# Kernel tuning notes

Measured on AMD Instinct MI355X. Metric: run time of the kernel, lower is better.

The kernel has to match this reference:

```python
import jax, jax.numpy as jnp
import numpy as np

HEAD_NUM = 8
QKV_DIM = 16
SQRT_EMBEDDING_DIM = 11.313708498984761  # sqrt(128)
LOGIT_CLIPPING = 10.0


def _reshape_by_heads(x):
    # x: [B, n, H*D] -> [B, H, n, D]
    B, n, _ = x.shape
    return x.reshape(B, n, HEAD_NUM, QKV_DIM).transpose(0, 2, 1, 3)


def setup_inputs() -> dict:
    key = jax.random.key(0)
    ks = jax.random.split(key, 12)
    B, P, N, E = 64, 500, 501, 128
    HD = HEAD_NUM * QKV_DIM
    s = 0.05
    return {
        "encoded_last_node": jax.random.normal(ks[0], (B, P, E), jnp.float32),
        "load": jax.random.uniform(ks[1], (B, P), jnp.float32),
        "ninf_mask": jnp.zeros((B, P, N), jnp.float32),
        "encoded_nodes": jax.random.normal(ks[2], (B, N, E), jnp.float32),
        "Wq_last": jax.random.normal(ks[3], (E + 1, HD), jnp.float32) * s,
        "Wk": jax.random.normal(ks[4], (E, HD), jnp.float32) * s,
        "Wv": jax.random.normal(ks[5], (E, HD), jnp.float32) * s,
        "mhc_W": jax.random.normal(ks[6], (HD, E), jnp.float32) * s,
        "mhc_b": jax.random.normal(ks[7], (E,), jnp.float32) * s,
        "new": jax.random.normal(ks[8], (B, HD, HD), jnp.float32) * s,
        "new_bias": jax.random.normal(ks[9], (B, 1, HD), jnp.float32) * s,
        "new_2": jax.random.normal(ks[10], (B, HD, HD), jnp.float32) * s,
        "new_bias_2": jax.random.normal(ks[11], (B, 1, HD), jnp.float32) * s,
    }


def reference(encoded_last_node, load, ninf_mask, encoded_nodes,
              Wq_last, Wk, Wv, mhc_W, mhc_b,
              new, new_bias, new_2, new_bias_2):
    B, P, E = encoded_last_node.shape
    # set_kv
    k = _reshape_by_heads(encoded_nodes @ Wk)            # [B,H,N,D]
    v = _reshape_by_heads(encoded_nodes @ Wv)            # [B,H,N,D]
    single_head_key = encoded_nodes.transpose(0, 2, 1)   # [B,E,N]

    # q from (last node embedding, load)
    input_cat = jnp.concatenate([encoded_last_node, load[:, :, None]], axis=2)  # [B,P,E+1]
    q = _reshape_by_heads(input_cat @ Wq_last)           # [B,H,P,D]

    # multi-head attention
    score = jnp.einsum('bhpd,bhnd->bhpn', q, k) / jnp.sqrt(jnp.float32(QKV_DIM))
    score = score + ninf_mask[:, None, :, :]
    attn = jax.nn.softmax(score, axis=3)
    out = jnp.einsum('bhpn,bhnd->bhpd', attn, v)         # [B,H,P,D]
    out_concat = out.transpose(0, 2, 1, 3).reshape(B, P, HEAD_NUM * QKV_DIM)

    # per-batch affine + relu + residual
    residual = out_concat
    h = jax.nn.relu(jnp.matmul(out_concat, new) + new_bias)
    h = jnp.matmul(h, new_2) + new_bias_2 + residual

    mh_atten_out = h @ mhc_W + mhc_b                     # [B,P,E]

    score2 = jnp.matmul(mh_atten_out, single_head_key)   # [B,P,N]
    score_clipped = LOGIT_CLIPPING * jnp.tanh(score2 / SQRT_EMBEDDING_DIM)
    probs = jax.nn.softmax(score_clipped + ninf_mask, axis=2)
    return probs
```

## Files before the change

kernel.cpp:

```cpp
#include <hip/hip_runtime.h>
#include <hip/hip_bf16.h>
#include <math.h>

typedef float f4 __attribute__((ext_vector_type(4)));

#define BATCH 64
#define PP 500
#define NN 501

__global__ __launch_bounds__(256) void k_proj(
    const float* __restrict__ Xq,
    const float* __restrict__ Ld,
    const float* __restrict__ Xn,
    const float* __restrict__ Wq,
    const float* __restrict__ Wk, const float* __restrict__ Wv,
    float* __restrict__ Q, float* __restrict__ K_, float* __restrict__ V_)
{
  __shared__ float xs[64*132];
  const int t = threadIdx.x;
  const int tr = t >> 5, tc = t & 31;
  if (blockIdx.x < 500) {
    const int r0 = blockIdx.x * 64;
    for (int i = t; i < 64*32; i += 256) {
      int r = i >> 5, k4 = (i & 31) << 2;
      *(f4*)(xs + r*132 + k4) = *(const f4*)(Xq + (size_t)(r0+r)*128 + k4);
    }
    if (t < 64) xs[t*132 + 128] = Ld[r0 + t];
    __syncthreads();
    float acc[8][4];
    #pragma unroll
    for (int i = 0; i < 8; i++)
      #pragma unroll
      for (int c = 0; c < 4; c++) acc[i][c] = 0.f;
    for (int k4 = 0; k4 < 128; k4 += 4) {
      f4 x[8], w[4];
      #pragma unroll
      for (int j = 0; j < 4; j++) w[j] = *(const f4*)(Wq + (size_t)(k4+j)*128 + tc*4);
      #pragma unroll
      for (int i = 0; i < 8; i++) x[i] = *(const f4*)(xs + (tr*8+i)*132 + k4);
      #pragma unroll
      for (int i = 0; i < 8; i++)
        #pragma unroll
        for (int j = 0; j < 4; j++)
          #pragma unroll
          for (int c = 0; c < 4; c++)
            acc[i][c] += x[i][j] * w[j][c];
    }
    {
      f4 w = *(const f4*)(Wq + (size_t)128*128 + tc*4);
      #pragma unroll
      for (int i = 0; i < 8; i++) {
        float xv = xs[(tr*8+i)*132 + 128];
        #pragma unroll
        for (int c = 0; c < 4; c++) acc[i][c] += xv * w[c];
      }
    }
    #pragma unroll
    for (int i = 0; i < 8; i++) {
      f4 o;
      #pragma unroll
      for (int c = 0; c < 4; c++) o[c] = acc[i][c];
      *(f4*)(Q + (size_t)(r0 + tr*8 + i)*128 + tc*4) = o;
    }
  } else {
    const int r0 = (blockIdx.x - 500) * 64;
    for (int i = t; i < 64*32; i += 256) {
      int r = i >> 5, k4 = (i & 31) << 2;
      *(f4*)(xs + r*132 + k4) = *(const f4*)(Xn + (size_t)(r0+r)*128 + k4);
    }
    __syncthreads();
    float accK[8][4], accV[8][4];
    #pragma unroll
    for (int i = 0; i < 8; i++)
      #pragma unroll
      for (int c = 0; c < 4; c++) { accK[i][c] = 0.f; accV[i][c] = 0.f; }
    for (int k4 = 0; k4 < 128; k4 += 4) {
      f4 x[8], wk[4], wv[4];
      #pragma unroll
      for (int j = 0; j < 4; j++) {
        wk[j] = *(const f4*)(Wk + (size_t)(k4+j)*128 + tc*4);
        wv[j] = *(const f4*)(Wv + (size_t)(k4+j)*128 + tc*4);
      }
      #pragma unroll
      for (int i = 0; i < 8; i++) x[i] = *(const f4*)(xs + (tr*8+i)*132 + k4);
      #pragma unroll
      for (int i = 0; i < 8; i++)
        #pragma unroll
        for (int j = 0; j < 4; j++)
          #pragma unroll
          for (int c = 0; c < 4; c++) {
            accK[i][c] += x[i][j] * wk[j][c];
            accV[i][c] += x[i][j] * wv[j][c];
          }
    }
    #pragma unroll
    for (int i = 0; i < 8; i++) {
      f4 ok, ov;
      #pragma unroll
      for (int c = 0; c < 4; c++) { ok[c] = accK[i][c]; ov[c] = accV[i][c]; }
      *(f4*)(K_ + (size_t)(r0 + tr*8 + i)*128 + tc*4) = ok;
      *(f4*)(V_ + (size_t)(r0 + tr*8 + i)*128 + tc*4) = ov;
    }
  }
}

__global__ __launch_bounds__(256, 3) void k_attn(
    const float* __restrict__ Q, const float* __restrict__ K_, const float* __restrict__ V_,
    const float* __restrict__ Msk, float* __restrict__ OC)
{
  __shared__ float ks[32*128];
  __shared__ float vs[32*128];
  __shared__ float mkt[32*64];
  const int blk = blockIdx.x;
  const int b  = blk >> 3;
  const int pt = blk & 7;
  const int p0 = pt * 64;
  const int t = threadIdx.x;
  const int h    = t >> 5;
  const int rowA = t & 31;
  const int rowB = rowA + 32;
  const int pA = p0 + rowA;
  const int pB0 = p0 + rowB;
  const bool bvalid = pB0 < PP;
  const int pB = bvalid ? pB0 : (PP - 1);

  f4 qA0, qA1, qA2, qA3, qB0, qB1, qB2, qB3;
  {
    const float* qa = Q + ((size_t)b*PP + pA)*128 + h*16;
    qA0 = *(const f4*)(qa); qA1 = *(const f4*)(qa+4); qA2 = *(const f4*)(qa+8); qA3 = *(const f4*)(qa+12);
    const float* qb = Q + ((size_t)b*PP + pB)*128 + h*16;
    qB0 = *(const f4*)(qb); qB1 = *(const f4*)(qb+4); qB2 = *(const f4*)(qb+8); qB3 = *(const f4*)(qb+12);
  }

  float mA = -1e30f, lA = 0.f, mB = -1e30f, lB = 0.f;
  f4 oA0 = {0.f,0.f,0.f,0.f}, oA1 = oA0, oA2 = oA0, oA3 = oA0;
  f4 oB0 = oA0, oB1 = oA0, oB2 = oA0, oB3 = oA0;

  const int mr = t >> 3;
  const int nq = (t & 7) << 2;
  const float* gmA = Msk + ((size_t)b*PP + p0 + mr)*NN;
  const float* gmB = Msk + ((size_t)b*PP + min(p0 + mr + 32, PP-1))*NN;

  for (int c0 = 0; c0 < NN; c0 += 32) {
    __syncthreads();
    #pragma unroll
    for (int u = 0; u < 4; u++) {
      int i = t + u*256;
      int n = i >> 5, d4 = (i & 31) << 2;
      int ng = c0 + n;
      f4 kv = {0.f,0.f,0.f,0.f}, vv = {0.f,0.f,0.f,0.f};
      if (ng < NN) {
        kv = *(const f4*)(K_ + ((size_t)b*NN + ng)*128 + d4);
        vv = *(const f4*)(V_ + ((size_t)b*NN + ng)*128 + d4);
      }
      *(f4*)(ks + n*128 + d4) = kv;
      *(f4*)(vs + n*128 + d4) = vv;
    }
    #pragma unroll
    for (int j = 0; j < 4; j++) {
      int nn = c0 + nq + j;
      bool cv = nn < NN;
      float a  = cv ? gmA[nn] : -1e30f;
      float bb = cv ? gmB[nn] : -1e30f;
      mkt[(nq+j)*64 + mr]      = a;
      mkt[(nq+j)*64 + mr + 32] = bb;
    }
    __syncthreads();

    #pragma unroll
    for (int n = 0; n < 32; n++) {
      const float* kf = ks + n*128 + h*16;
      f4 k0 = *(const f4*)(kf);
      f4 k1 = *(const f4*)(kf + 4);
      f4 k2 = *(const f4*)(kf + 8);
      f4 k3 = *(const f4*)(kf + 12);
      float sA = 0.f, sB = 0.f;
      #pragma unroll
      for (int d = 0; d < 4; d++) {
        sA += qA0[d]*k0[d]; sB += qB0[d]*k0[d];
        sA += qA1[d]*k1[d]; sB += qB1[d]*k1[d];
        sA += qA2[d]*k2[d]; sB += qB2[d]*k2[d];
        sA += qA3[d]*k3[d]; sB += qB3[d]*k3[d];
      }
      sA = sA*0.25f + mkt[n*64 + rowA];
      sB = sB*0.25f + mkt[n*64 + rowB];
      if (sA > mA) {
        float cc = __expf(mA - sA); mA = sA; lA *= cc;
        oA0 *= cc; oA1 *= cc; oA2 *= cc; oA3 *= cc;
      }
      if (sB > mB) {
        float cc = __expf(mB - sB); mB = sB; lB *= cc;
        oB0 *= cc; oB1 *= cc; oB2 *= cc; oB3 *= cc;
      }
      float eA = __expf(sA - mA); lA += eA;
      float eB = __expf(sB - mB); lB += eB;
      const float* vf = vs + n*128 + h*16;
      f4 v0 = *(const f4*)(vf);
      f4 v1 = *(const f4*)(vf + 4);
      f4 v2 = *(const f4*)(vf + 8);
      f4 v3 = *(const f4*)(vf + 12);
      oA0 += eA*v0; oA1 += eA*v1; oA2 += eA*v2; oA3 += eA*v3;
      oB0 += eB*v0; oB1 += eB*v1; oB2 += eB*v2; oB3 += eB*v3;
    }
  }

  {
    float inv = 1.f / lA;
    float* orow = OC + ((size_t)b*PP + pA)*128 + h*16;
    *(f4*)(orow)      = oA0 * inv;
    *(f4*)(orow + 4)  = oA1 * inv;
    *(f4*)(orow + 8)  = oA2 * inv;
    *(f4*)(orow + 12) = oA3 * inv;
  }
  if (bvalid) {
    float inv = 1.f / lB;
    float* orow = OC + ((size_t)b*PP + pB)*128 + h*16;
    *(f4*)(orow)      = oB0 * inv;
    *(f4*)(orow + 4)  = oB1 * inv;
    *(f4*)(orow + 8)  = oB2 * inv;
    *(f4*)(orow + 12) = oB3 * inv;
  }
}

__global__ __launch_bounds__(256) void k_ffn(
    const float* __restrict__ OC, const float* __restrict__ Wn, const float* __restrict__ Bn,
    const float* __restrict__ Wn2, const float* __restrict__ Bn2,
    const float* __restrict__ Wm, const float* __restrict__ Bm,
    float* __restrict__ MH)
{
  __shared__ float xs[64*132];
  __shared__ float hs[64*132];
  const int blk = blockIdx.x; const int b = blk >> 3, rb = blk & 7;
  const int r0 = rb*64;
  const int nv = min(64, PP - r0);
  const int t = threadIdx.x;
  const int tr = t >> 5, tc = t & 31;
  const float* ocb = OC + (size_t)b*PP*128;
  for (int i = t; i < 64*32; i += 256) {
    int r = i >> 5, k4 = (i & 31) << 2;
    f4 v = {0.f,0.f,0.f,0.f};
    if (r < nv) v = *(const f4*)(ocb + (size_t)(r0+r)*128 + k4);
    *(f4*)(xs + r*132 + k4) = v;
  }
  __syncthreads();
  {
    const float* W1 = Wn + (size_t)b*16384;
    float acc[8][4];
    #pragma unroll
    for (int i = 0; i < 8; i++)
      #pragma unroll
      for (int c = 0; c < 4; c++) acc[i][c] = 0.f;
    for (int k4 = 0; k4 < 128; k4 += 4) {
      f4 x[8], w[4];
      #pragma unroll
      for (int j = 0; j < 4; j++) w[j] = *(const f4*)(W1 + (size_t)(k4+j)*128 + tc*4);
      #pragma unroll
      for (int i = 0; i < 8; i++) x[i] = *(const f4*)(xs + (tr*8+i)*132 + k4);
      #pragma unroll
      for (int i = 0; i < 8; i++)
        #pragma unroll
        for (int j = 0; j < 4; j++)
          #pragma unroll
          for (int c = 0; c < 4; c++)
            acc[i][c] += x[i][j] * w[j][c];
    }
    f4 b1 = *(const f4*)(Bn + b*128 + tc*4);
    #pragma unroll
    for (int i = 0; i < 8; i++) {
      f4 o;
      #pragma unroll
      for (int c = 0; c < 4; c++) o[c] = fmaxf(acc[i][c] + b1[c], 0.f);
      *(f4*)(hs + (tr*8+i)*132 + tc*4) = o;
    }
  }
  __syncthreads();
  float h2[8][4];
  {
    const float* W2 = Wn2 + (size_t)b*16384;
    float acc[8][4];
    #pragma unroll
    for (int i = 0; i < 8; i++)
      #pragma unroll
      for (int c = 0; c < 4; c++) acc[i][c] = 0.f;
    for (int k4 = 0; k4 < 128; k4 += 4) {
      f4 x[8], w[4];
      #pragma unroll
      for (int j = 0; j < 4; j++) w[j] = *(const f4*)(W2 + (size_t)(k4+j)*128 + tc*4);
      #pragma unroll
      for (int i = 0; i < 8; i++) x[i] = *(const f4*)(hs + (tr*8+i)*132 + k4);
      #pragma unroll
      for (int i = 0; i < 8; i++)
        #pragma unroll
        for (int j = 0; j < 4; j++)
          #pragma unroll
          for (int c = 0; c < 4; c++)
            acc[i][c] += x[i][j] * w[j][c];
    }
    f4 b2 = *(const f4*)(Bn2 + b*128 + tc*4);
    #pragma unroll
    for (int i = 0; i < 8; i++)
      #pragma unroll
      for (int c = 0; c < 4; c++)
        h2[i][c] = acc[i][c] + b2[c] + xs[(tr*8+i)*132 + tc*4 + c];
  }
  __syncthreads();
  #pragma unroll
  for (int i = 0; i < 8; i++) {
    f4 o;
    #pragma unroll
    for (int c = 0; c < 4; c++) o[c] = h2[i][c];
    *(f4*)(hs + (tr*8+i)*132 + tc*4) = o;
  }
  __syncthreads();
  {
    float acc[8][4];
    #pragma unroll
    for (int i = 0; i < 8; i++)
      #pragma unroll
      for (int c = 0; c < 4; c++) acc[i][c] = 0.f;
    for (int k4 = 0; k4 < 128; k4 += 4) {
      f4 x[8], w[4];
      #pragma unroll
      for (int j = 0; j < 4; j++) w[j] = *(const f4*)(Wm + (size_t)(k4+j)*128 + tc*4);
      #pragma unroll
      for (int i = 0; i < 8; i++) x[i] = *(const f4*)(hs + (tr*8+i)*132 + k4);
      #pragma unroll
      for (int i = 0; i < 8; i++)
        #pragma unroll
        for (int j = 0; j < 4; j++)
          #pragma unroll
          for (int c = 0; c < 4; c++)
            acc[i][c] += x[i][j] * w[j][c];
    }
    f4 b3 = *(const f4*)(Bm + tc*4);
    #pragma unroll
    for (int i = 0; i < 8; i++) {
      if (tr*8 + i < nv) {
        f4 o;
        #pragma unroll
        for (int c = 0; c < 4; c++) o[c] = acc[i][c] + b3[c];
        *(f4*)(MH + ((size_t)b*PP + r0 + tr*8 + i)*128 + tc*4) = o;
      }
    }
  }
}

__global__ __launch_bounds__(256, 3) void k_final(
    const float* __restrict__ MH, const float* __restrict__ EN,
    const float* __restrict__ Msk, float* __restrict__ OUT)
{
  __shared__ float ms[32*132];
  __shared__ float es[64*132];
  const int blk = blockIdx.x; const int b = blk >> 4, rb = blk & 15;
  const int r0 = rb*32; const int nv = min(32, PP - r0);
  const int t = threadIdx.x;
  const int tr = t >> 5, tc = t & 31;
  const float* mhb = MH + (size_t)(b*PP + r0)*128;
  for (int i = t; i < 32*32; i += 256) {
    int r = i >> 5, k4 = (i & 31) << 2;
    f4 v = {0.f,0.f,0.f,0.f};
    if (r < nv) v = *(const f4*)(mhb + (size_t)r*128 + k4);
    *(f4*)(ms + r*132 + k4) = v;
  }
  const float* enb = EN + (size_t)b*NN*128;
  float s[8][4][2];
  #pragma unroll
  for (int nt = 0; nt < 8; nt++) {
    const int n0 = nt*64;
    __syncthreads();
    for (int i = t; i < 64*32; i += 256) {
      int n = i >> 5, k4 = (i & 31) << 2;
      f4 v = {0.f,0.f,0.f,0.f};
      if (n0 + n < NN) v = *(const f4*)(enb + (size_t)(n0+n)*128 + k4);
      *(f4*)(es + n*132 + k4) = v;
    }
    __syncthreads();
    float acc[4][2];
    #pragma unroll
    for (int i = 0; i < 4; i++) { acc[i][0] = 0.f; acc[i][1] = 0.f; }
    #pragma unroll 8
    for (int k4 = 0; k4 < 128; k4 += 4) {
      f4 x[4];
      #pragma unroll
      for (int i = 0; i < 4; i++) x[i] = *(const f4*)(ms + (tr*4+i)*132 + k4);
      f4 e0 = *(const f4*)(es + tc*132 + k4);
      f4 e1 = *(const f4*)(es + (tc+32)*132 + k4);
      #pragma unroll
      for (int i = 0; i < 4; i++)
        #pragma unroll
        for (int j = 0; j < 4; j++) {
          acc[i][0] += x[i][j]*e0[j];
          acc[i][1] += x[i][j]*e1[j];
        }
    }
    #pragma unroll
    for (int i = 0; i < 4; i++) {
      s[nt][i][0] = acc[i][0];
      s[nt][i][1] = acc[i][1];
    }
  }
  const float* mkb = Msk + (size_t)(b*PP + r0)*NN;
  #pragma unroll
  for (int nt = 0; nt < 8; nt++)
    #pragma unroll
    for (int i = 0; i < 4; i++)
      #pragma unroll
      for (int c = 0; c < 2; c++) {
        int r = tr*4 + i, n = nt*64 + tc + c*32;
        float val = -INFINITY;
        if (r < nv && n < NN) {
          float E = __expf(s[nt][i][c] * 0.17677669529663687f);
          val = 10.f - 20.f/(E + 1.f) + mkb[(size_t)r*NN + n];
        }
        s[nt][i][c] = val;
      }
  float* ob = OUT + (size_t)(b*PP + r0)*NN;
  #pragma unroll
  for (int i = 0; i < 4; i++) {
    float m = -INFINITY;
    #pragma unroll
    for (int nt = 0; nt < 8; nt++)
      #pragma unroll
      for (int c = 0; c < 2; c++) m = fmaxf(m, s[nt][i][c]);
    #pragma unroll
    for (int o = 16; o > 0; o >>= 1) m = fmaxf(m, __shfl_xor(m, o, 32));
    float l = 0.f;
    #pragma unroll
    for (int nt = 0; nt < 8; nt++)
      #pragma unroll
      for (int c = 0; c < 2; c++) {
        float e_ = __expf(s[nt][i][c] - m);
        s[nt][i][c] = e_;
        l += e_;
      }
    #pragma unroll
    for (int o = 16; o > 0; o >>= 1) l += __shfl_xor(l, o, 32);
    const int r = tr*4 + i;
    if (r < nv) {
      float inv = 1.f / l;
      float* orow = ob + (size_t)r*NN;
      #pragma unroll
      for (int nt = 0; nt < 8; nt++)
        #pragma unroll
        for (int c = 0; c < 2; c++) {
          int n = nt*64 + tc + c*32;
          if (n < NN) orow[n] = s[nt][i][c] * inv;
        }
    }
  }
}

extern "C" void kernel_launch(void* const* d_in, const int* in_sizes, int n_in,
                              void* d_out, int out_size, void* d_ws, size_t ws_size,
                              hipStream_t stream) {
  const float* eln  = (const float*)d_in[0];
  const float* load = (const float*)d_in[1];
  const float* mask = (const float*)d_in[2];
  const float* en   = (const float*)d_in[3];
  const float* Wq   = (const float*)d_in[4];
  const float* Wk   = (const float*)d_in[5];
  const float* Wv   = (const float*)d_in[6];
  const float* Wm   = (const float*)d_in[7];
  const float* Bm   = (const float*)d_in[8];
  const float* Wn   = (const float*)d_in[9];
  const float* Bn   = (const float*)d_in[10];
  const float* Wn2  = (const float*)d_in[11];
  const float* Bn2  = (const float*)d_in[12];
  float* out = (float*)d_out;
  float* ws  = (float*)d_ws;
  float* Q   = ws;
  float* K_  = ws + 4096000;
  float* V_  = ws + 8200192;
  float* OC  = ws + 12304384;
  float* MH  = ws + 16400384;
  hipLaunchKernelGGL(k_proj,  dim3(1001), dim3(256), 0, stream, eln, load, en, Wq, Wk, Wv, Q, K_, V_);
  hipLaunchKernelGGL(k_attn,  dim3(512),  dim3(256), 0, stream, Q, K_, V_, mask, OC);
  hipLaunchKernelGGL(k_ffn,   dim3(512),  dim3(256), 0, stream, OC, Wn, Bn, Wn2, Bn2, Wm, Bm, MH);
  hipLaunchKernelGGL(k_final, dim3(1024), dim3(256), 0, stream, MH, en, mask, out);
}
```

Baseline: 472.0 us.

## Register-prefetch next K/V/mask tile in attention loop and repad mask smem

```diff
diff --git a/kernel.cpp b/kernel.cpp
--- a/kernel.cpp
+++ b/kernel.cpp
@@ -104,23 +104,23 @@
   }
 }
 
-__global__ __launch_bounds__(256, 3) void k_attn(
+__global__ __launch_bounds__(256, 2) void k_attn(
     const float* __restrict__ Q, const float* __restrict__ K_, const float* __restrict__ V_,
     const float* __restrict__ Msk, float* __restrict__ OC)
 {
   __shared__ float ks[32*128];
   __shared__ float vs[32*128];
-  __shared__ float mkt[32*64];
+  __shared__ float mks[64*33];
   const int blk = blockIdx.x;
   const int b  = blk >> 3;
   const int pt = blk & 7;
   const int p0 = pt * 64;
   const int t = threadIdx.x;
-  const int h    = t >> 5;
-  const int rowA = t & 31;
-  const int rowB = rowA + 32;
-  const int pA = p0 + rowA;
-  const int pB0 = p0 + rowB;
+  const int h  = t >> 5;
+  const int rA = t & 31;
+  const int rB = rA + 32;
+  const int pA = p0 + rA;
+  const int pB0 = p0 + rB;
   const bool bvalid = pB0 < PP;
   const int pB = bvalid ? pB0 : (PP - 1);
 
@@ -136,40 +136,64 @@
   f4 oA0 = {0.f,0.f,0.f,0.f}, oA1 = oA0, oA2 = oA0, oA3 = oA0;
   f4 oB0 = oA0, oB1 = oA0, oB2 = oA0, oB3 = oA0;
 
-  const int mr = t >> 3;
-  const int nq = (t & 7) << 2;
-  const float* gmA = Msk + ((size_t)b*PP + p0 + mr)*NN;
-  const float* gmB = Msk + ((size_t)b*PP + min(p0 + mr + 32, PP-1))*NN;
+  const int mr2 = t >> 2;
+  const int nq2 = (t & 3) << 3;
+  const int mrow = min(p0 + mr2, PP - 1);
+  const float* gm = Msk + ((size_t)b*PP + mrow)*NN;
+
+  f4 kpre[4], vpre[4]; float mpre[8];
+  #pragma unroll
+  for (int u = 0; u < 4; u++) {
+    int i = t + u*256;
+    int n = i >> 5, d4 = (i & 31) << 2;
+    kpre[u] = *(const f4*)(K_ + ((size_t)b*NN + n)*128 + d4);
+    vpre[u] = *(const f4*)(V_ + ((size_t)b*NN + n)*128 + d4);
+  }
+  #pragma unroll
+  for (int j = 0; j < 8; j++)
+    mpre[j] = (nq2 + j < NN) ? gm[nq2 + j] : -1e30f;
 
   for (int c0 = 0; c0 < NN; c0 += 32) {
-    __syncthreads();
     #pragma unroll
     for (int u = 0; u < 4; u++) {
       int i = t + u*256;
       int n = i >> 5, d4 = (i & 31) << 2;
-      int ng = c0 + n;
-      f4 kv = {0.f,0.f,0.f,0.f}, vv = {0.f,0.f,0.f,0.f};
-      if (ng < NN) {
-        kv = *(const f4*)(K_ + ((size_t)b*NN + ng)*128 + d4);
-        vv = *(const f4*)(V_ + ((size_t)b*NN + ng)*128 + d4);
-      }
-      *(f4*)(ks + n*128 + d4) = kv;
-      *(f4*)(vs + n*128 + d4) = vv;
-    }
-    #pragma unroll
-    for (int j = 0; j < 4; j++) {
-      int nn = c0 + nq + j;
-      bool cv = nn < NN;
-      float a  = cv ? gmA[nn] : -1e30f;
-      float bb = cv ? gmB[nn] : -1e30f;
-      mkt[(nq+j)*64 + mr]      = a;
-      mkt[(nq+j)*64 + mr + 32] = bb;
+      *(f4*)(ks + n*128 + d4) = kpre[u];
+      *(f4*)(vs + n*128 + d4) = vpre[u];
+    }
+    {
+      float* dm = mks + mr2*33 + nq2;
+      #pragma unroll
+      for (int j = 0; j < 8; j++) dm[j] = mpre[j];
     }
     __syncthreads();
 
+    const int c1 = c0 + 32;
+    if (c1 < NN) {
+      #pragma unroll
+      for (int u = 0; u < 4; u++) {
+        int i = t + u*256;
+        int n = i >> 5, d4 = (i & 31) << 2;
+        int ng = c1 + n;
+        f4 kv = {0.f,0.f,0.f,0.f}, vv = {0.f,0.f,0.f,0.f};
+        if (ng < NN) {
+          kv = *(const f4*)(K_ + ((size_t)b*NN + ng)*128 + d4);
+          vv = *(const f4*)(V_ + ((size_t)b*NN + ng)*128 + d4);
+        }
+        kpre[u] = kv; vpre[u] = vv;
+      }
+      #pragma unroll
+      for (int j = 0; j < 8; j++)
+        mpre[j] = (c1 + nq2 + j < NN) ? gm[c1 + nq2 + j] : -1e30f;
+    }
+
+    const float* ksh = ks + h*16;
+    const float* vsh = vs + h*16;
+    const float* mwA = mks + rA*33;
+    const float* mwB = mks + rB*33;
     #pragma unroll
     for (int n = 0; n < 32; n++) {
-      const float* kf = ks + n*128 + h*16;
+      const float* kf = ksh + n*128;
       f4 k0 = *(const f4*)(kf);
       f4 k1 = *(const f4*)(kf + 4);
       f4 k2 = *(const f4*)(kf + 8);
@@ -182,8 +206,8 @@
         sA += qA2[d]*k2[d]; sB += qB2[d]*k2[d];
         sA += qA3[d]*k3[d]; sB += qB3[d]*k3[d];
       }
-      sA = sA*0.25f + mkt[n*64 + rowA];
-      sB = sB*0.25f + mkt[n*64 + rowB];
+      sA = sA*0.25f + mwA[n];
+      sB = sB*0.25f + mwB[n];
       if (sA > mA) {
         float cc = __expf(mA - sA); mA = sA; lA *= cc;
         oA0 *= cc; oA1 *= cc; oA2 *= cc; oA3 *= cc;
@@ -194,7 +218,7 @@
       }
       float eA = __expf(sA - mA); lA += eA;
       float eB = __expf(sB - mB); lB += eB;
-      const float* vf = vs + n*128 + h*16;
+      const float* vf = vsh + n*128;
       f4 v0 = *(const f4*)(vf);
       f4 v1 = *(const f4*)(vf + 4);
       f4 v2 = *(const f4*)(vf + 8);
@@ -202,6 +226,7 @@
       oA0 += eA*v0; oA1 += eA*v1; oA2 += eA*v2; oA3 += eA*v3;
       oB0 += eB*v0; oB1 += eB*v1; oB2 += eB*v2; oB3 += eB*v3;
     }
+    __syncthreads();
   }
 
   {
```

New measurement: 442.6 us. 1.07x faster.
